# Performance work log

Hardware: AMD Instinct MI355X
Metric: run time of the kernel (lower is better)

Reference implementation:

```python
import jax, jax.numpy as jnp
import numpy as np
from jax import lax

IMG = 512            # image H = W
FH = FW = 32         # feature map spatial size
A = 9                # anchors per location (3 sizes x 3 ratios)
N = FH * FW * A      # total anchors = 9216
IOU_THR = 0.7
MIN_SCORE = 0.5
MIN_SIZE = 1e-3


def make_anchors():
    """Anchors in centroid format (cx, cy, w, h), ordered (H, W, A)."""
    stride = IMG / FH
    sizes = np.array([32.0, 64.0, 128.0])
    ratios = np.array([0.5, 1.0, 2.0])
    ws = (sizes[:, None] / np.sqrt(ratios)[None, :]).reshape(-1)  # (A,)
    hs = (sizes[:, None] * np.sqrt(ratios)[None, :]).reshape(-1)  # (A,)
    cx = (np.arange(FW) + 0.5) * stride
    cy = (np.arange(FH) + 0.5) * stride
    CX = np.broadcast_to(cx[None, :, None], (FH, FW, A))
    CY = np.broadcast_to(cy[:, None, None], (FH, FW, A))
    Wg = np.broadcast_to(ws[None, None, :], (FH, FW, A))
    Hg = np.broadcast_to(hs[None, None, :], (FH, FW, A))
    anc = np.stack([CX, CY, Wg, Hg], axis=-1).reshape(-1, 4)
    return jnp.asarray(anc, dtype=jnp.float32)


def pairwise_iou(b):
    # b: (N,4) corners x1,y1,x2,y2
    x1, y1, x2, y2 = b[:, 0], b[:, 1], b[:, 2], b[:, 3]
    area = (x2 - x1) * (y2 - y1)
    ix1 = jnp.maximum(x1[:, None], x1[None, :])
    iy1 = jnp.maximum(y1[:, None], y1[None, :])
    ix2 = jnp.minimum(x2[:, None], x2[None, :])
    iy2 = jnp.minimum(y2[:, None], y2[None, :])
    inter = jnp.maximum(ix2 - ix1, 0.0) * jnp.maximum(iy2 - iy1, 0.0)
    union = area[:, None] + area[None, :] - inter
    return inter / jnp.maximum(union, 1e-9)


def nms_keep(boxes, scores, valid):
    """Greedy NMS. Returns bool keep mask of shape (N,). Index decisions only."""
    s = jnp.where(valid, scores, -jnp.inf)
    order = jnp.argsort(-s)
    b = boxes[order]
    v = valid[order]
    ious = pairwise_iou(b)  # (N, N)
    idx = jnp.arange(N)

    def body(i, supp):
        keep_i = (~supp[i]) & v[i]
        return supp | (keep_i & (ious[i] > IOU_THR) & (idx > i))

    supp = lax.fori_loop(0, N, body, jnp.zeros(N, dtype=bool))
    keep_sorted = (~supp) & v
    return jnp.zeros(N, dtype=bool).at[order].set(keep_sorted)


def setup_inputs() -> dict:
    key = jax.random.key(0)
    ks = jax.random.split(key, 4)
    return {
        "feature_map": jax.random.normal(ks[0], (1, 256, FH, FW), jnp.float32),
        "conv1_w": jax.random.normal(ks[1], (512, 256, 3, 3), jnp.float32) * 0.02,
        "conv1_b": jnp.zeros((512,), jnp.float32),
        "conv2_w": jax.random.normal(ks[2], (A, 512), jnp.float32) * 0.01,
        "conv2_b": jnp.zeros((A,), jnp.float32),
        "conv3_w": jax.random.normal(ks[3], (4 * A, 512), jnp.float32) * 0.01,
        "conv3_b": jnp.zeros((4 * A,), jnp.float32),
    }


def reference(feature_map, conv1_w, conv1_b, conv2_w, conv2_b, conv3_w, conv3_b):
    anchors = make_anchors()  # (N,4) cx,cy,w,h

    # --- conv backbone head ---
    h = lax.conv_general_dilated(
        feature_map, conv1_w, (1, 1), "SAME",
        dimension_numbers=("NCHW", "OIHW", "NCHW"))
    h = jax.nn.relu(h + conv1_b[None, :, None, None])  # (1,512,H,W)

    scores = jax.nn.sigmoid(
        jnp.einsum("bchw,ac->bahw", h, conv2_w) + conv2_b[None, :, None, None])
    scores = scores.transpose(0, 2, 3, 1).reshape(-1)  # (N,) ordered (H,W,A)

    off = jnp.einsum("bchw,oc->bohw", h, conv3_w) + conv3_b[None, :, None, None]
    off = off.reshape(1, A, 4, FH, FW).transpose(0, 3, 4, 1, 2).reshape(-1, 4)

    acx, acy, aw, ah = anchors[:, 0], anchors[:, 1], anchors[:, 2], anchors[:, 3]
    cx = acx + off[:, 0] * aw
    cy = acy + off[:, 1] * ah
    bw = aw * jnp.exp(off[:, 2])
    bh = ah * jnp.exp(off[:, 3])
    boxes = jnp.stack([cx - bw / 2, cy - bh / 2, cx + bw / 2, cy + bh / 2], axis=1)

    # --- clip to image ---
    lo = jnp.array([0.0, 0.0, 0.0, 0.0], jnp.float32)
    hi = jnp.array([IMG, IMG, IMG, IMG], jnp.float32)
    boxes = jnp.clip(boxes, lo, hi)

    # --- remove small boxes + score threshold (as a mask, jit-safe) ---
    valid = ((boxes[:, 2] - boxes[:, 0]) >= MIN_SIZE) \
          & ((boxes[:, 3] - boxes[:, 1]) >= MIN_SIZE) \
          & (scores >= MIN_SCORE)

    # --- NMS (selection is index-based; no gradient through the decision) ---
    keep = nms_keep(lax.stop_gradient(boxes), lax.stop_gradient(scores), valid)

    out = jnp.concatenate(
        [boxes * keep[:, None].astype(boxes.dtype),
         (scores * keep.astype(scores.dtype))[:, None]], axis=1)  # (N,5)
    return out
```

## Files before the change

kernel.cpp:

```cpp
#include <hip/hip_runtime.h>
#include <math.h>

#define FHW   32
#define NA    9
#define NBOX  9216
#define C1    256
#define C2    512
#define KTOT  2304
#define BK    16
#define CAP   64
#define CAPL  4

struct AnchorWH { float w[NA]; float h[NA]; };

#define FP_OFF    0u
#define WT_OFF    1183744u
#define HP_OFF    5902336u

__global__ __launch_bounds__(256) void k_prep(const float* __restrict__ fin,
                                              float* __restrict__ Fp,
                                              unsigned int* __restrict__ deg,
                                              unsigned int* __restrict__ nv,
                                              const float* __restrict__ w1,
                                              float* __restrict__ Wt,
                                              float* __restrict__ out) {
    if (blockIdx.x < 1156) {
        int idx = blockIdx.x * 256 + threadIdx.x;
        if (idx < 256 * 34 * 34) {
            int c   = idx / 1156;
            int rem = idx - c * 1156;
            int yy  = rem / 34;
            int xx  = rem - yy * 34;
            float v = 0.f;
            if (yy >= 1 && yy <= 32 && xx >= 1 && xx <= 32)
                v = fin[c * 1024 + (yy - 1) * 32 + (xx - 1)];
            Fp[idx] = v;
        }
        if (idx < NBOX)     deg[idx] = 0u;
        if (idx < NBOX * 5) out[idx] = 0.f;
        if (idx == 0)       *nv = 0u;
    } else {
        __shared__ float tile[32][33];
        int tb  = blockIdx.x - 1156;
        int k0  = (tb % 72) * 32;
        int oc0 = (tb / 72) * 32;
        int t   = threadIdx.x;
        int r0 = t >> 5, c = t & 31;
        #pragma unroll
        for (int i = 0; i < 4; ++i) {
            int r = r0 + 8 * i;
            tile[r][c] = w1[(oc0 + r) * KTOT + k0 + c];
        }
        __syncthreads();
        #pragma unroll
        for (int i = 0; i < 4; ++i) {
            int kk  = r0 + 8 * i;
            int k   = k0 + kk;
            int ch  = k / 9;
            int kap = k - ch * 9;
            Wt[(kap * 256 + ch) * C2 + oc0 + c] = tile[c][kk];
        }
    }
}

__global__ __launch_bounds__(256) void k_gemm(const float* __restrict__ Fp,
                                              const float* __restrict__ Wt,
                                              float* __restrict__ hp,
                                              int kshift) {
    const int KCHd  = KTOT >> kshift;
    const int NTd   = KCHd >> 4;
    const int kmask = (1 << kshift) - 1;
    const int id = blockIdx.x;
    const int kz = id & kmask;
    const int g  = id >> kshift;
    const int by = g & 3, bx = g >> 2;
    const int p0  = bx * 128;
    const int oc0 = by * 128;
    const int k0b = kz * KCHd;
    const int t  = threadIdx.x;
    const int ty = t >> 4, tx = t & 15;

    __shared__ float As[BK][128];
    __shared__ float Bs[BK][128];

    const int pp  = t & 127;
    const int th  = t >> 7;
    const int pyx = ((p0 + pp) >> 5) * 34 + ((p0 + pp) & 31);
    const int rB  = t >> 5;
    const int cB  = (t & 31) * 4;

    float acc[2][2][4][4];
    #pragma unroll
    for (int rh = 0; rh < 2; ++rh)
        #pragma unroll
        for (int ch = 0; ch < 2; ++ch)
            #pragma unroll
            for (int r = 0; r < 4; ++r)
                #pragma unroll
                for (int c = 0; c < 4; ++c) acc[rh][ch][r][c] = 0.f;

    float  aS[8];
    float4 bS0, bS1;

    auto LOAD = [&](int s) {
        int tap = s >> 8, c0 = s & 255;
        int dy  = (tap * 11) >> 5;
        int dx  = tap - 3 * dy;
        const float* ab = Fp + ((c0 + th) * 34 + dy) * 34 + dx + pyx;
        #pragma unroll
        for (int i = 0; i < 8; ++i) aS[i] = ab[i * 2312];
        const float* bb = Wt + (s + rB) * C2 + oc0 + cB;
        bS0 = *(const float4*)bb;
        bS1 = *(const float4*)(bb + 8 * C2);
    };
    auto STORE = [&]() {
        #pragma unroll
        for (int i = 0; i < 8; ++i) As[2 * i + th][pp] = aS[i];
        *(float4*)&Bs[rB][cB]     = bS0;
        *(float4*)&Bs[rB + 8][cB] = bS1;
    };

    LOAD(k0b);
    #pragma unroll 1
    for (int tile = 0; tile < NTd; ++tile) {
        __syncthreads();
        STORE();
        __syncthreads();
        if (tile + 1 < NTd) LOAD(k0b + (tile + 1) * BK);
        #pragma unroll
        for (int kk = 0; kk < BK; ++kk) {
            float a[2][4], b[2][4];
            *(float4*)&a[0][0] = *(const float4*)&As[kk][ty * 4];
            *(float4*)&a[1][0] = *(const float4*)&As[kk][ty * 4 + 64];
            *(float4*)&b[0][0] = *(const float4*)&Bs[kk][tx * 4];
            *(float4*)&b[1][0] = *(const float4*)&Bs[kk][tx * 4 + 64];
            #pragma unroll
            for (int rh = 0; rh < 2; ++rh)
                #pragma unroll
                for (int ch = 0; ch < 2; ++ch)
                    #pragma unroll
                    for (int r = 0; r < 4; ++r)
                        #pragma unroll
                        for (int c = 0; c < 4; ++c)
                            acc[rh][ch][r][c] = fmaf(a[rh][r], b[ch][c], acc[rh][ch][r][c]);
        }
    }

    #pragma unroll
    for (int rh = 0; rh < 2; ++rh)
        #pragma unroll
        for (int r = 0; r < 4; ++r) {
            int p = p0 + rh * 64 + ty * 4 + r;
            float* dst = hp + ((size_t)(kz * 1024 + p)) * C2 + oc0 + tx * 4;
            *(float4*)dst        = *(float4*)&acc[rh][0][r][0];
            *(float4*)(dst + 64) = *(float4*)&acc[rh][1][r][0];
        }
}

__global__ __launch_bounds__(256) void k_heads(const float* __restrict__ hp,
                                               const float* __restrict__ b1,
                                               const float* __restrict__ w2,
                                               const float* __restrict__ b2,
                                               const float* __restrict__ w3,
                                               const float* __restrict__ b3,
                                               float* __restrict__ boxes,
                                               float* __restrict__ scoresG,
                                               unsigned int* __restrict__ nv,
                                               unsigned int* __restrict__ vlist,
                                               AnchorWH awh, int KSd) {
    const int p0 = blockIdx.x * 4;
    const int t  = threadIdx.x;
    __shared__ float hrow[4][C2];
    __shared__ float arr[4][45];

    {
        const int c4 = t & 127;
        const int ph = t >> 7;
        #pragma unroll
        for (int px2 = 0; px2 < 2; ++px2) {
            int px = px2 * 2 + ph;
            int p  = p0 + px;
            float4 s = ((const float4*)b1)[c4];
            for (int ks = 0; ks < KSd; ++ks) {
                float4 v = ((const float4*)hp)[(size_t)(ks * 1024 + p) * 128 + c4];
                s.x += v.x; s.y += v.y; s.z += v.z; s.w += v.w;
            }
            s.x = fmaxf(s.x, 0.f); s.y = fmaxf(s.y, 0.f);
            s.z = fmaxf(s.z, 0.f); s.w = fmaxf(s.w, 0.f);
            *(float4*)&hrow[px][c4 * 4] = s;
        }
    }
    __syncthreads();

    {
        const int grp = t >> 4, l = t & 15;
        for (int r = 0; r < 12; ++r) {
            int j180 = grp + (r << 4);
            float s = 0.f;
            int px = 0, j = 0;
            if (j180 < 180) {
                px = j180 / 45; j = j180 - px * 45;
                const float* wp = (j < 9) ? (w2 + j * C2) : (w3 + (j - 9) * C2);
                #pragma unroll
                for (int i = 0; i < 32; ++i)
                    s += hrow[px][l + 16 * i] * wp[l + 16 * i];
            }
            s += __shfl_xor(s, 1, 16);
            s += __shfl_xor(s, 2, 16);
            s += __shfl_xor(s, 4, 16);
            s += __shfl_xor(s, 8, 16);
            if (j180 < 180 && l == 0) arr[px][j] = s;
        }
    }
    __syncthreads();

    if (t < 36) {
        int px = t / 9, a = t - px * 9;
        int p = p0 + px;
        float logit = arr[px][a] + b2[a];
        float score = 1.f / (1.f + expf(-logit));
        float o0 = arr[px][9 + a * 4 + 0] + b3[a * 4 + 0];
        float o1 = arr[px][9 + a * 4 + 1] + b3[a * 4 + 1];
        float o2 = arr[px][9 + a * 4 + 2] + b3[a * 4 + 2];
        float o3 = arr[px][9 + a * 4 + 3] + b3[a * 4 + 3];
        int y = p >> 5, x = p & 31;
        float ax = (x + 0.5f) * 16.f, ay = (y + 0.5f) * 16.f;
        float aw = awh.w[a], ah = awh.h[a];
        float cx = ax + o0 * aw;
        float cy = ay + o1 * ah;
        float bw = aw * expf(o2);
        float bh = ah * expf(o3);
        float x1 = fminf(fmaxf(cx - bw * 0.5f, 0.f), 512.f);
        float y1 = fminf(fmaxf(cy - bh * 0.5f, 0.f), 512.f);
        float x2 = fminf(fmaxf(cx + bw * 0.5f, 0.f), 512.f);
        float y2 = fminf(fmaxf(cy + bh * 0.5f, 0.f), 512.f);
        int n = p * 9 + a;
        float4 bx4; bx4.x = x1; bx4.y = y1; bx4.z = x2; bx4.w = y2;
        ((float4*)boxes)[n] = bx4;
        scoresG[n] = score;
        bool valid = (x2 - x1 >= 0.001f) && (y2 - y1 >= 0.001f) && (score >= 0.5f);
        if (valid) {
            unsigned int ci = atomicAdd(nv, 1u);
            vlist[ci] = (unsigned int)n;
        }
    }
}

__global__ __launch_bounds__(256) void k_adj(const unsigned int* __restrict__ nvp,
                                             const unsigned int* __restrict__ vlist,
                                             const float* __restrict__ boxes,
                                             const float* __restrict__ scoresG,
                                             unsigned int* __restrict__ deg,
                                             unsigned short* __restrict__ adj) {
    const int Nv = (int)*nvp;
    const int T  = (Nv + 127) >> 7;
    const int NP = T * (T + 1) / 2;
    int t = threadIdx.x;

    __shared__ float4 ub[128], vb[128];
    __shared__ float  us[128], vs[128];
    __shared__ int    uo[128], vo[128];

    for (int b = blockIdx.x; b < NP; b += gridDim.x) {
        int tv = (int)(sqrtf(2.f * b + 0.25f) - 0.5f);
        while ((tv + 1) * (tv + 2) / 2 <= b) tv++;
        while (tv * (tv + 1) / 2 > b) tv--;
        int tu = b - tv * (tv + 1) / 2;

        if (t < 128) {
            int gi = tu * 128 + t;
            if (gi < Nv) { int n = (int)vlist[gi]; ub[t] = ((const float4*)boxes)[n]; us[t] = scoresG[n]; uo[t] = n; }
            else us[t] = -1.f;
        } else {
            int tt = t - 128;
            int gj = tv * 128 + tt;
            if (gj < Nv) { int n = (int)vlist[gj]; vb[tt] = ((const float4*)boxes)[n]; vs[tt] = scoresG[n]; vo[tt] = n; }
            else vs[tt] = -1.f;
        }
        __syncthreads();

        for (int s = 0; s < 64; ++s) {
            int q  = t + 256 * s;
            int i  = q >> 7, jj = q & 127;
            if (tu == tv && i >= jj) continue;
            float su = us[i], sv = vs[jj];
            if (su < 0.f || sv < 0.f) continue;
            float4 bu = ub[i], bv = vb[jj];
            float au = (bu.z - bu.x) * (bu.w - bu.y);
            float av = (bv.z - bv.x) * (bv.w - bv.y);
            float ix1 = fmaxf(bu.x, bv.x), iy1 = fmaxf(bu.y, bv.y);
            float ix2 = fminf(bu.z, bv.z), iy2 = fminf(bu.w, bv.w);
            float inter = fmaxf(ix2 - ix1, 0.f) * fmaxf(iy2 - iy1, 0.f);
            float uni = au + av - inter;
            float iou = inter / fmaxf(uni, 1e-9f);
            if (iou > 0.7f) {
                int gi = tu * 128 + i, gj = tv * 128 + jj;
                bool uHigh = (su > sv) || (su == sv && uo[i] < vo[jj]);
                int hi = uHigh ? gi : gj;
                int lo = uHigh ? gj : gi;
                unsigned int old = atomicAdd(&deg[hi], 1u);
                if ((old & 0xFFFFu) < CAP) {
                    adj[hi * CAP + (old & 0xFFFFu)] = (unsigned short)lo;
                    atomicAdd(&deg[lo], 0x10000u);
                }
            }
        }
        __syncthreads();
    }
}

__global__ __launch_bounds__(512) void k_peel(const unsigned int* __restrict__ nvp,
                                              const unsigned int* __restrict__ vlist,
                                              const unsigned int* __restrict__ degG,
                                              const unsigned short* __restrict__ adjG,
                                              const float* __restrict__ boxes,
                                              const float* __restrict__ scoresG,
                                              float* __restrict__ out) {
    __shared__ unsigned int   word[NBOX];
    __shared__ unsigned char  st[NBOX];
    __shared__ unsigned char  doutL[NBOX];
    __shared__ unsigned short outL[NBOX * CAPL];
    const int t  = threadIdx.x;
    const int Nv = (int)*nvp;
    const int chunk = (Nv + 511) / 512;
    const int i0 = t * chunk;
    const int i1 = (i0 + chunk < Nv) ? (i0 + chunk) : Nv;

    unsigned int amask = 0, smask = 0;
    for (int i = i0; i < i1; ++i) {
        unsigned int dg = degG[i];
        unsigned int cin = dg >> 16;
        int dout = (int)(dg & 0xFFFFu); if (dout > CAP) dout = CAP;
        doutL[i] = (unsigned char)dout;
        int dl = (dout < CAPL) ? dout : CAPL;
        for (int s = 0; s < dl; ++s)
            outL[i * CAPL + s] = adjG[i * CAP + s];
        word[i] = cin;
        st[i] = 0;
        if (cin == 0u) smask |= 1u << (i - i0);
        else           amask |= 1u << (i - i0);
    }
    __syncthreads();

    auto PUSH = [&](int i, bool kept) {
        int dout = (int)doutL[i];
        unsigned int delta = kept ? 0xFFFFu : 0xFFFFFFFFu;
        for (int s = 0; s < dout; ++s) {
            int j = (s < CAPL) ? (int)outL[i * CAPL + s]
                               : (int)adjG[i * CAP + s];
            atomicAdd(&word[j], delta);
        }
    };

    {
        unsigned int m = smask;
        while (m) {
            int b = __ffs(m) - 1; m &= m - 1;
            int i = i0 + b;
            st[i] = 1;
            PUSH(i, true);
        }
    }

    {
        volatile unsigned int* vw = word;
        int idle = 0;
        while (__any(amask != 0u)) {
            bool prog = false;
            unsigned int m = amask;
            while (m) {
                int b = __ffs(m) - 1; m &= m - 1;
                int i = i0 + b;
                unsigned int w = vw[i];
                if ((w & 0xFFFFu) == 0u) {
                    bool kept = (w >> 16) == 0u;
                    st[i] = kept ? 1 : 2;
                    PUSH(i, kept);
                    amask &= ~(1u << b);
                    prog = true;
                }
            }
            if (__any(prog)) idle = 0;
            else {
                ++idle;
                if (idle > 8000) break;
                if (idle > 2) __builtin_amdgcn_s_sleep(1);
            }
        }
    }
    __syncthreads();

    for (int i = i0; i < i1; ++i) {
        if (st[i] == 1) {
            int n = (int)vlist[i];
            float4 b = ((const float4*)boxes)[n];
            out[n * 5 + 0] = b.x;
            out[n * 5 + 1] = b.y;
            out[n * 5 + 2] = b.z;
            out[n * 5 + 3] = b.w;
            out[n * 5 + 4] = scoresG[n];
        }
    }
}

extern "C" void kernel_launch(void* const* d_in, const int* in_sizes, int n_in,
                              void* d_out, int out_size, void* d_ws, size_t ws_size,
                              hipStream_t stream) {
    const float* fin = (const float*)d_in[0];
    const float* w1  = (const float*)d_in[1];
    const float* b1  = (const float*)d_in[2];
    const float* w2  = (const float*)d_in[3];
    const float* b2  = (const float*)d_in[4];
    const float* w3  = (const float*)d_in[5];
    const float* b3  = (const float*)d_in[6];
    float* out = (float*)d_out;

    const size_t need16 = (size_t)HP_OFF + 33554432u
                        + 147456u + 3u * 36864u + 1179648u + 256u;
    int kshift = (ws_size >= need16) ? 4 : 3;
    int KSd = 1 << kshift;
    size_t hpB = (size_t)KSd * 1024 * C2 * 4;

    char* ws = (char*)d_ws;
    float*          Fp    = (float*)(ws + FP_OFF);
    float*          Wt    = (float*)(ws + WT_OFF);
    float*          hp    = (float*)(ws + HP_OFF);
    size_t o = HP_OFF + hpB;
    float*          boxes = (float*)(ws + o); o += (size_t)NBOX * 16;
    float*          sc    = (float*)(ws + o); o += (size_t)NBOX * 4;
    unsigned int*   vlist = (unsigned int*)(ws + o); o += (size_t)NBOX * 4;
    unsigned int*   deg   = (unsigned int*)(ws + o); o += (size_t)NBOX * 4;
    unsigned short* adj   = (unsigned short*)(ws + o); o += (size_t)NBOX * CAP * 2;
    unsigned int*   nv    = (unsigned int*)(ws + o);

    AnchorWH awh;
    {
        const double sizes[3]  = {32.0, 64.0, 128.0};
        const double ratios[3] = {0.5, 1.0, 2.0};
        for (int si = 0; si < 3; ++si)
            for (int ri = 0; ri < 3; ++ri) {
                awh.w[si * 3 + ri] = (float)(sizes[si] / sqrt(ratios[ri]));
                awh.h[si * 3 + ri] = (float)(sizes[si] * sqrt(ratios[ri]));
            }
    }

    k_prep<<<dim3(1156 + 72 * 16), 256, 0, stream>>>(fin, Fp, deg, nv, w1, Wt, out);
    k_gemm<<<dim3(32 * KSd), 256, 0, stream>>>(Fp, Wt, hp, kshift);
    k_heads<<<dim3(256), 256, 0, stream>>>(hp, b1, w2, b2, w3, b3, boxes, sc, nv, vlist, awh, KSd);
    k_adj<<<dim3(512), 256, 0, stream>>>(nv, vlist, boxes, sc, deg, adj);
    k_peel<<<dim3(1), 512, 0, stream>>>(nv, vlist, deg, adj, boxes, sc, out);
}
```

Before: 189.4 us.

## Replace polling NMS peel with single-wave worklist queue, fix split-K at 8

```diff
diff --git a/kernel.cpp b/kernel.cpp
--- a/kernel.cpp
+++ b/kernel.cpp
@@ -7,7 +7,10 @@
 #define C1    256
 #define C2    512
 #define KTOT  2304
+#define KS    8
+#define KCH   (KTOT / KS)
 #define BK    16
+#define NT    (KCH / BK)
 #define CAP   64
 #define CAPL  4
 
@@ -16,6 +19,12 @@
 #define FP_OFF    0u
 #define WT_OFF    1183744u
 #define HP_OFF    5902336u
+#define BOX_OFF   22679552u
+#define SC_OFF    22827008u
+#define VL_OFF    22863872u
+#define DEG_OFF   22900736u
+#define ADJ_OFF   22937600u
+#define NV_OFF    24117248u
 
 __global__ __launch_bounds__(256) void k_prep(const float* __restrict__ fin,
                                               float* __restrict__ Fp,
@@ -65,18 +74,14 @@
 
 __global__ __launch_bounds__(256) void k_gemm(const float* __restrict__ Fp,
                                               const float* __restrict__ Wt,
-                                              float* __restrict__ hp,
-                                              int kshift) {
-    const int KCHd  = KTOT >> kshift;
-    const int NTd   = KCHd >> 4;
-    const int kmask = (1 << kshift) - 1;
+                                              float* __restrict__ hp) {
     const int id = blockIdx.x;
-    const int kz = id & kmask;
-    const int g  = id >> kshift;
+    const int kz = id & 7;
+    const int g  = id >> 3;
     const int by = g & 3, bx = g >> 2;
     const int p0  = bx * 128;
     const int oc0 = by * 128;
-    const int k0b = kz * KCHd;
+    const int k0b = kz * KCH;
     const int t  = threadIdx.x;
     const int ty = t >> 4, tx = t & 15;
 
@@ -122,11 +127,11 @@
 
     LOAD(k0b);
     #pragma unroll 1
-    for (int tile = 0; tile < NTd; ++tile) {
+    for (int tile = 0; tile < NT; ++tile) {
         __syncthreads();
         STORE();
         __syncthreads();
-        if (tile + 1 < NTd) LOAD(k0b + (tile + 1) * BK);
+        if (tile + 1 < NT) LOAD(k0b + (tile + 1) * BK);
         #pragma unroll
         for (int kk = 0; kk < BK; ++kk) {
             float a[2][4], b[2][4];
@@ -167,7 +172,7 @@
                                                float* __restrict__ scoresG,
                                                unsigned int* __restrict__ nv,
                                                unsigned int* __restrict__ vlist,
-                                               AnchorWH awh, int KSd) {
+                                               AnchorWH awh) {
     const int p0 = blockIdx.x * 4;
     const int t  = threadIdx.x;
     __shared__ float hrow[4][C2];
@@ -181,7 +186,8 @@
             int px = px2 * 2 + ph;
             int p  = p0 + px;
             float4 s = ((const float4*)b1)[c4];
-            for (int ks = 0; ks < KSd; ++ks) {
+            #pragma unroll
+            for (int ks = 0; ks < KS; ++ks) {
                 float4 v = ((const float4*)hp)[(size_t)(ks * 1024 + p) * 128 + c4];
                 s.x += v.x; s.y += v.y; s.z += v.z; s.w += v.w;
             }
@@ -320,13 +326,17 @@
     __shared__ unsigned char  st[NBOX];
     __shared__ unsigned char  doutL[NBOX];
     __shared__ unsigned short outL[NBOX * CAPL];
+    __shared__ unsigned short qbuf[NBOX];
+    __shared__ unsigned int   qw;
     const int t  = threadIdx.x;
     const int Nv = (int)*nvp;
     const int chunk = (Nv + 511) / 512;
     const int i0 = t * chunk;
     const int i1 = (i0 + chunk < Nv) ? (i0 + chunk) : Nv;
 
-    unsigned int amask = 0, smask = 0;
+    if (t == 0) qw = 0u;
+    __syncthreads();
+
     for (int i = i0; i < i1; ++i) {
         unsigned int dg = degG[i];
         unsigned int cin = dg >> 16;
@@ -336,56 +346,47 @@
         for (int s = 0; s < dl; ++s)
             outL[i * CAPL + s] = adjG[i * CAP + s];
         word[i] = cin;
-        st[i] = 0;
-        if (cin == 0u) smask |= 1u << (i - i0);
-        else           amask |= 1u << (i - i0);
+        if (cin == 0u) {
+            st[i] = 1;
+            unsigned int slot = atomicAdd(&qw, 1u);
+            qbuf[slot] = (unsigned short)(i | 0x8000);
+        } else {
+            st[i] = 0;
+        }
     }
     __syncthreads();
 
-    auto PUSH = [&](int i, bool kept) {
-        int dout = (int)doutL[i];
-        unsigned int delta = kept ? 0xFFFFu : 0xFFFFFFFFu;
-        for (int s = 0; s < dout; ++s) {
-            int j = (s < CAPL) ? (int)outL[i * CAPL + s]
-                               : (int)adjG[i * CAP + s];
-            atomicAdd(&word[j], delta);
-        }
-    };
-
-    {
-        unsigned int m = smask;
-        while (m) {
-            int b = __ffs(m) - 1; m &= m - 1;
-            int i = i0 + b;
-            st[i] = 1;
-            PUSH(i, true);
-        }
-    }
-
-    {
-        volatile unsigned int* vw = word;
-        int idle = 0;
-        while (__any(amask != 0u)) {
-            bool prog = false;
-            unsigned int m = amask;
-            while (m) {
-                int b = __ffs(m) - 1; m &= m - 1;
-                int i = i0 + b;
-                unsigned int w = vw[i];
-                if ((w & 0xFFFFu) == 0u) {
-                    bool kept = (w >> 16) == 0u;
-                    st[i] = kept ? 1 : 2;
-                    PUSH(i, kept);
-                    amask &= ~(1u << b);
-                    prog = true;
+    if (t < 64) {
+        volatile unsigned int* vqw = &qw;
+        int qr = 0;
+        long guard = 0;
+        while (qr < Nv) {
+            int avail = (int)(*vqw) - qr;
+            if (avail <= 0) {
+                if (++guard > 4000000) break;
+                continue;
+            }
+            int take = (avail < 64) ? avail : 64;
+            if (t < take) {
+                unsigned short e = qbuf[qr + t];
+                int j      = (int)(e & 0x3FFFu);
+                bool kept  = (e & 0x8000u) != 0;
+                int dout = (int)doutL[j];
+                unsigned int delta = kept ? 0xFFFFu : 0xFFFFFFFFu;
+                for (int s = 0; s < dout; ++s) {
+                    int tg = (s < CAPL) ? (int)outL[j * CAPL + s]
+                                        : (int)adjG[j * CAP + s];
+                    unsigned int old = atomicAdd(&word[tg], delta);
+                    if ((old & 0xFFFFu) == 1u) {
+                        unsigned int sup = (old >> 16) + (kept ? 1u : 0u);
+                        bool k2 = (sup == 0u);
+                        st[tg] = k2 ? 1 : 2;
+                        unsigned int slot = atomicAdd(&qw, 1u);
+                        qbuf[slot] = (unsigned short)(tg | (k2 ? 0x8000u : 0u));
+                    }
                 }
             }
-            if (__any(prog)) idle = 0;
-            else {
-                ++idle;
-                if (idle > 8000) break;
-                if (idle > 2) __builtin_amdgcn_s_sleep(1);
-            }
+            qr += take;
         }
     }
     __syncthreads();
@@ -415,23 +416,16 @@
     const float* b3  = (const float*)d_in[6];
     float* out = (float*)d_out;
 
-    const size_t need16 = (size_t)HP_OFF + 33554432u
-                        + 147456u + 3u * 36864u + 1179648u + 256u;
-    int kshift = (ws_size >= need16) ? 4 : 3;
-    int KSd = 1 << kshift;
-    size_t hpB = (size_t)KSd * 1024 * C2 * 4;
-
     char* ws = (char*)d_ws;
     float*          Fp    = (float*)(ws + FP_OFF);
     float*          Wt    = (float*)(ws + WT_OFF);
     float*          hp    = (float*)(ws + HP_OFF);
-    size_t o = HP_OFF + hpB;
-    float*          boxes = (float*)(ws + o); o += (size_t)NBOX * 16;
-    float*          sc    = (float*)(ws + o); o += (size_t)NBOX * 4;
-    unsigned int*   vlist = (unsigned int*)(ws + o); o += (size_t)NBOX * 4;
-    unsigned int*   deg   = (unsigned int*)(ws + o); o += (size_t)NBOX * 4;
-    unsigned short* adj   = (unsigned short*)(ws + o); o += (size_t)NBOX * CAP * 2;
-    unsigned int*   nv    = (unsigned int*)(ws + o);
+    float*          boxes = (float*)(ws + BOX_OFF);
+    float*          sc    = (float*)(ws + SC_OFF);
+    unsigned int*   vlist = (unsigned int*)(ws + VL_OFF);
+    unsigned int*   deg   = (unsigned int*)(ws + DEG_OFF);
+    unsigned short* adj   = (unsigned short*)(ws + ADJ_OFF);
+    unsigned int*   nv    = (unsigned int*)(ws + NV_OFF);
 
     AnchorWH awh;
     {
@@ -445,8 +439,8 @@
     }
 
     k_prep<<<dim3(1156 + 72 * 16), 256, 0, stream>>>(fin, Fp, deg, nv, w1, Wt, out);
-    k_gemm<<<dim3(32 * KSd), 256, 0, stream>>>(Fp, Wt, hp, kshift);
-    k_heads<<<dim3(256), 256, 0, stream>>>(hp, b1, w2, b2, w3, b3, boxes, sc, nv, vlist, awh, KSd);
+    k_gemm<<<dim3(256), 256, 0, stream>>>(Fp, Wt, hp);
+    k_heads<<<dim3(256), 256, 0, stream>>>(hp, b1, w2, b2, w3, b3, boxes, sc, nv, vlist, awh);
     k_adj<<<dim3(512), 256, 0, stream>>>(nv, vlist, boxes, sc, deg, adj);
     k_peel<<<dim3(1), 512, 0, stream>>>(nv, vlist, deg, adj, boxes, sc, out);
 }
```

After: 274.3 us. +44.8%, slower.
